# Performance work log

Hardware: AMD Instinct MI355X
Metric: run time of the kernel (lower is better)

Reference implementation:

```python
import jax, jax.numpy as jnp
import numpy as np

N_EMBED = 1024
HEAD_SIZE = 128
B, T = 8, 2048


def setup_inputs() -> dict:
    key = jax.random.key(0)
    kx, kk, kq, kv = jax.random.split(key, 4)
    x = jax.random.normal(kx, (B, T, N_EMBED), dtype=jnp.float32)
    Wk = jax.random.normal(kk, (N_EMBED, HEAD_SIZE), dtype=jnp.float32) * (N_EMBED ** -0.5)
    Wq = jax.random.normal(kq, (N_EMBED, HEAD_SIZE), dtype=jnp.float32) * (N_EMBED ** -0.5)
    Wv = jax.random.normal(kv, (N_EMBED, HEAD_SIZE), dtype=jnp.float32) * (N_EMBED ** -0.5)
    return {"x": x, "Wk": Wk, "Wq": Wq, "Wv": Wv}


def reference(x, Wk, Wq, Wv):
    # x: [B, T, C]; single-head causal attention, dropout rate 0 (identity)
    t = x.shape[1]
    k = jnp.einsum("btc,ch->bth", x, Wk)  # keys
    q = jnp.einsum("btc,ch->bth", x, Wq)  # queries
    v = jnp.einsum("btc,ch->bth", x, Wv)  # values
    scale = k.shape[-1] ** -0.5
    scores = jnp.einsum("bqh,bkh->bqk", q, k) * scale  # [B, T, T]
    causal = jnp.tril(jnp.ones((t, t), dtype=bool))
    scores = jnp.where(causal, scores, -jnp.inf)
    attn = jax.nn.softmax(scores, axis=-1)
    return jnp.einsum("bqk,bkh->bqh", attn, v)
```

## Files before the change

### kernel.cpp

```cpp
#include <hip/hip_runtime.h>
#include <hip/hip_bf16.h>
#include <math.h>

#define B_ 8
#define T_ 2048
#define C_ 1024
#define D_ 128
#define M_ (B_*T_)

typedef __attribute__((ext_vector_type(8))) short short8;
typedef __attribute__((ext_vector_type(4))) float floatx4;
typedef __hip_bfloat16 bf16;

#define QSCALE 0.12751744416218247f

__global__ __launch_bounds__(256) void cvt_w2_kernel(const float* __restrict__ Wq,
                                                     const float* __restrict__ Wk,
                                                     const float* __restrict__ Wv,
                                                     bf16* __restrict__ Wt) {
    __shared__ bf16 tl[64][136];
    const int t = threadIdx.x;
    const int k0 = blockIdx.x * 64, g = blockIdx.y;
    const float* W = (g == 0) ? Wq : (g == 1) ? Wk : Wv;
    {
        int k = t >> 2, n0 = (t & 3) * 32;
        const float* src = W + (size_t)(k0 + k) * 128 + n0;
#pragma unroll
        for (int j = 0; j < 4; ++j) {
            float4 v0 = *(const float4*)(src + j * 8);
            float4 v1 = *(const float4*)(src + j * 8 + 4);
            union { short8 s; __hip_bfloat162 h[4]; } u;
            __hip_bfloat162 h;
            h.x = __float2bfloat16(v0.x); h.y = __float2bfloat16(v0.y); u.h[0] = h;
            h.x = __float2bfloat16(v0.z); h.y = __float2bfloat16(v0.w); u.h[1] = h;
            h.x = __float2bfloat16(v1.x); h.y = __float2bfloat16(v1.y); u.h[2] = h;
            h.x = __float2bfloat16(v1.z); h.y = __float2bfloat16(v1.w); u.h[3] = h;
            *(short8*)&tl[k][n0 + j * 8] = u.s;
        }
    }
    __syncthreads();
    {
        int n = t >> 1, ko = (t & 1) * 32;
        union { short8 s[4]; bf16 e[32]; } u;
#pragma unroll
        for (int i = 0; i < 32; ++i) u.e[i] = tl[ko + i][n];
        bf16* dst = Wt + (size_t)g * 131072 + (size_t)n * 1024 + k0 + ko;
#pragma unroll
        for (int j = 0; j < 4; ++j) *(short8*)(dst + j * 8) = u.s[j];
    }
}

__global__ __launch_bounds__(256, 3) void proj4_kernel(const float* __restrict__ x,
                                                       const bf16* __restrict__ Wt,
                                                       bf16* __restrict__ Qb,
                                                       bf16* __restrict__ Kb,
                                                       bf16* __restrict__ Vt) {
    __shared__ bf16 la[64][72];
    __shared__ bf16 lb[256][72];
    const int t = threadIdx.x;
    const int wave = t >> 6, lane = t & 63;
    const int quad = lane >> 4, l15 = lane & 15;
    const int row0 = (blockIdx.x >> 1) * 64;
    const int path = blockIdx.x & 1;
    const int ar = t >> 2, ao = (t & 3) * 16;

    if (path == 0) {
        floatx4 acc[4][4];
#pragma unroll
        for (int m = 0; m < 4; ++m)
#pragma unroll
            for (int n = 0; n < 4; ++n) acc[m][n] = (floatx4)0.0f;

        for (int kc = 0; kc < 16; ++kc) {
            {
                const float* src = x + (size_t)(row0 + ar) * 1024 + kc * 64 + ao;
                float4 v0 = *(const float4*)src;
                float4 v1 = *(const float4*)(src + 4);
                float4 v2 = *(const float4*)(src + 8);
                float4 v3 = *(const float4*)(src + 12);
                union { short8 s; __hip_bfloat162 h[4]; } u0, u1;
                __hip_bfloat162 h;
                h.x = __float2bfloat16(v0.x); h.y = __float2bfloat16(v0.y); u0.h[0] = h;
                h.x = __float2bfloat16(v0.z); h.y = __float2bfloat16(v0.w); u0.h[1] = h;
                h.x = __float2bfloat16(v1.x); h.y = __float2bfloat16(v1.y); u0.h[2] = h;
                h.x = __float2bfloat16(v1.z); h.y = __float2bfloat16(v1.w); u0.h[3] = h;
                h.x = __float2bfloat16(v2.x); h.y = __float2bfloat16(v2.y); u1.h[0] = h;
                h.x = __float2bfloat16(v2.z); h.y = __float2bfloat16(v2.w); u1.h[1] = h;
                h.x = __float2bfloat16(v3.x); h.y = __float2bfloat16(v3.y); u1.h[2] = h;
                h.x = __float2bfloat16(v3.z); h.y = __float2bfloat16(v3.w); u1.h[3] = h;
                *(short8*)&la[ar][ao] = u0.s;
                *(short8*)&la[ar][ao + 8] = u1.s;
            }
#pragma unroll
            for (int j = 0; j < 8; ++j) {
                int c = t + j * 256;
                int rb = c >> 3, ob = (c & 7) * 8;
                int g = rb >> 7, n = rb & 127;
                *(short8*)&lb[rb][ob] = *(const short8*)(Wt + (size_t)g * 131072 + (size_t)n * 1024 + kc * 64 + ob);
            }
            __syncthreads();
#pragma unroll
            for (int dk = 0; dk < 2; ++dk) {
                short8 af[4], bff[4];
#pragma unroll
                for (int m = 0; m < 4; ++m) af[m] = *(const short8*)&la[m * 16 + l15][dk * 32 + quad * 8];
#pragma unroll
                for (int n = 0; n < 4; ++n) bff[n] = *(const short8*)&lb[wave * 64 + n * 16 + l15][dk * 32 + quad * 8];
#pragma unroll
                for (int m = 0; m < 4; ++m)
#pragma unroll
                    for (int n = 0; n < 4; ++n)
                        acc[m][n] = __builtin_amdgcn_mfma_f32_16x16x32_bf16(af[m], bff[n], acc[m][n], 0, 0, 0);
            }
            __syncthreads();
        }

        bf16* outp = (wave < 2) ? Qb : Kb;
        const float qs = (wave < 2) ? QSCALE : 1.0f;
        const int cb = (wave & 1) * 64;
#pragma unroll
        for (int m = 0; m < 4; ++m)
#pragma unroll
            for (int r = 0; r < 4; ++r) {
                int row = row0 + m * 16 + quad * 4 + r;
#pragma unroll
                for (int n = 0; n < 4; ++n)
                    outp[(size_t)row * 128 + cb + n * 16 + l15] = __float2bfloat16(acc[m][n][r] * qs);
            }
    } else {
        const int wr = wave >> 1, wc = wave & 1;
        floatx4 acc[2][4];
#pragma unroll
        for (int m = 0; m < 2; ++m)
#pragma unroll
            for (int n = 0; n < 4; ++n) acc[m][n] = (floatx4)0.0f;

        for (int kc = 0; kc < 16; ++kc) {
            {
                const float* src = x + (size_t)(row0 + ar) * 1024 + kc * 64 + ao;
                float4 v0 = *(const float4*)src;
                float4 v1 = *(const float4*)(src + 4);
                float4 v2 = *(const float4*)(src + 8);
                float4 v3 = *(const float4*)(src + 12);
                union { short8 s; __hip_bfloat162 h[4]; } u0, u1;
                __hip_bfloat162 h;
                h.x = __float2bfloat16(v0.x); h.y = __float2bfloat16(v0.y); u0.h[0] = h;
                h.x = __float2bfloat16(v0.z); h.y = __float2bfloat16(v0.w); u0.h[1] = h;
                h.x = __float2bfloat16(v1.x); h.y = __float2bfloat16(v1.y); u0.h[2] = h;
                h.x = __float2bfloat16(v1.z); h.y = __float2bfloat16(v1.w); u0.h[3] = h;
                h.x = __float2bfloat16(v2.x); h.y = __float2bfloat16(v2.y); u1.h[0] = h;
                h.x = __float2bfloat16(v2.z); h.y = __float2bfloat16(v2.w); u1.h[1] = h;
                h.x = __float2bfloat16(v3.x); h.y = __float2bfloat16(v3.y); u1.h[2] = h;
                h.x = __float2bfloat16(v3.z); h.y = __float2bfloat16(v3.w); u1.h[3] = h;
                *(short8*)&la[ar][ao] = u0.s;
                *(short8*)&la[ar][ao + 8] = u1.s;
            }
#pragma unroll
            for (int j = 0; j < 4; ++j) {
                int c = t + j * 256;
                int rb = c >> 3, ob = (c & 7) * 8;
                *(short8*)&lb[rb][ob] = *(const short8*)(Wt + 2 * 131072 + (size_t)rb * 1024 + kc * 64 + ob);
            }
            __syncthreads();
#pragma unroll
            for (int dk = 0; dk < 2; ++dk) {
                short8 af[2], bff[4];
#pragma unroll
                for (int m = 0; m < 2; ++m) af[m] = *(const short8*)&la[wr * 32 + m * 16 + l15][dk * 32 + quad * 8];
#pragma unroll
                for (int n = 0; n < 4; ++n) bff[n] = *(const short8*)&lb[wc * 64 + n * 16 + l15][dk * 32 + quad * 8];
#pragma unroll
                for (int m = 0; m < 2; ++m)
#pragma unroll
                    for (int n = 0; n < 4; ++n)
                        acc[m][n] = __builtin_amdgcn_mfma_f32_16x16x32_bf16(af[m], bff[n], acc[m][n], 0, 0, 0);
            }
            __syncthreads();
        }

        bf16* vtl = &lb[0][0];
#pragma unroll
        for (int m = 0; m < 2; ++m)
#pragma unroll
            for (int r = 0; r < 4; ++r) {
                int tt = wr * 32 + m * 16 + quad * 4 + r;
#pragma unroll
                for (int n = 0; n < 4; ++n)
                    vtl[tt * 136 + wc * 64 + n * 16 + l15] = __float2bfloat16(acc[m][n][r]);
            }
        __syncthreads();
        {
            int d = t >> 1, toff = (t & 1) * 32;
            union { short8 s[4]; bf16 e[32]; } u;
#pragma unroll
            for (int i = 0; i < 32; ++i) u.e[i] = vtl[(toff + i) * 136 + d];
            int bb = row0 >> 11, t0 = row0 & 2047;
            bf16* dst = Vt + (size_t)(bb * D_ + d) * T_ + t0 + toff;
#pragma unroll
            for (int j = 0; j < 4; ++j) *(short8*)(dst + j * 8) = u.s[j];
        }
    }
}

__global__ __launch_bounds__(256, 3) void flash_fm2_kernel(const bf16* __restrict__ Qb,
                                                           const bf16* __restrict__ Kb,
                                                           const bf16* __restrict__ Vt,
                                                           float* __restrict__ out,
                                                           bf16* __restrict__ Opart,
                                                           float* __restrict__ Lpart) {
    const int tile = blockIdx.x, seg = blockIdx.y, b = blockIdx.z;
    const int keys_total = (tile + 1) * 64;
    const int nseg = (keys_total + 255) >> 8;
    if (seg >= nseg) return;

    __shared__ bf16 lds_k[64][136];
    __shared__ bf16 lds_v[128][72];
    __shared__ bf16 lds_p[4][16][72];
    const int t = threadIdx.x;
    const int wave = t >> 6, lane = t & 63;
    const int quad = lane >> 4, l15 = lane & 15;
    const int q0 = tile * 64;
    const int k_start = seg << 8;
    const int k_end = min(k_start + 256, keys_total);
    const int nch = (k_end - k_start) >> 6;

    short8 qf[4];
    {
        int qm = q0 + wave * 16 + l15;
#pragma unroll
        for (int dk = 0; dk < 4; ++dk)
            qf[dk] = *(const short8*)(Qb + (size_t)(b * T_ + qm) * 128 + dk * 32 + quad * 8);
    }

    short8 kreg[4], vreg[4];
    {
        const int k0 = k_start;
#pragma unroll
        for (int j = 0; j < 4; ++j) {
            int c = t + j * 256;
            { int r = c >> 4, co = (c & 15) * 8;
              kreg[j] = *(const short8*)(Kb + (size_t)(b * T_ + k0 + r) * 128 + co); }
            { int d = c >> 3, co = (c & 7) * 8;
              vreg[j] = *(const short8*)(Vt + (size_t)b * (D_ * T_) + d * T_ + k0 + co); }
        }
    }

    floatx4 o_acc[8];
#pragma unroll
    for (int i = 0; i < 8; ++i) o_acc[i] = (floatx4)0.0f;
    float lp[4] = {0.f, 0.f, 0.f, 0.f};
    const int qrow = q0 + wave * 16 + quad * 4;

    for (int ch = 0; ch < nch; ++ch) {
        const int k0 = k_start + (ch << 6);
        __syncthreads();
#pragma unroll
        for (int j = 0; j < 4; ++j) {
            int c = t + j * 256;
            { int r = c >> 4, co = (c & 15) * 8; *(short8*)&lds_k[r][co] = kreg[j]; }
            { int d = c >> 3, co = (c & 7) * 8;  *(short8*)&lds_v[d][co] = vreg[j]; }
        }
        if (ch + 1 < nch) {
            const int kn = k0 + 64;
#pragma unroll
            for (int j = 0; j < 4; ++j) {
                int c = t + j * 256;
                { int r = c >> 4, co = (c & 15) * 8;
                  kreg[j] = *(const short8*)(Kb + (size_t)(b * T_ + kn + r) * 128 + co); }
                { int d = c >> 3, co = (c & 7) * 8;
                  vreg[j] = *(const short8*)(Vt + (size_t)b * (D_ * T_) + d * T_ + kn + co); }
            }
        }
        __syncthreads();

        floatx4 s[4];
#pragma unroll
        for (int nt = 0; nt < 4; ++nt) s[nt] = (floatx4)0.0f;
#pragma unroll
        for (int dk = 0; dk < 4; ++dk)
#pragma unroll
            for (int nt = 0; nt < 4; ++nt) {
                short8 kb = *(const short8*)&lds_k[nt * 16 + l15][dk * 32 + quad * 8];
                s[nt] = __builtin_amdgcn_mfma_f32_16x16x32_bf16(qf[dk], kb, s[nt], 0, 0, 0);
            }

        float sv[4][4];
#pragma unroll
        for (int nt = 0; nt < 4; ++nt)
#pragma unroll
            for (int r = 0; r < 4; ++r) sv[nt][r] = s[nt][r];

        if (k0 + 63 > q0) {
#pragma unroll
            for (int nt = 0; nt < 4; ++nt) {
                int key = k0 + nt * 16 + l15;
#pragma unroll
                for (int r = 0; r < 4; ++r)
                    if (key > qrow + r) sv[nt][r] = -1e30f;
            }
        }

#pragma unroll
        for (int nt = 0; nt < 4; ++nt)
#pragma unroll
            for (int r = 0; r < 4; ++r) sv[nt][r] = exp2f(sv[nt][r]);
#pragma unroll
        for (int r = 0; r < 4; ++r)
            lp[r] += (sv[0][r] + sv[1][r]) + (sv[2][r] + sv[3][r]);

#pragma unroll
        for (int nt = 0; nt < 4; ++nt)
#pragma unroll
            for (int r = 0; r < 4; ++r)
                lds_p[wave][quad * 4 + r][nt * 16 + l15] = __float2bfloat16(sv[nt][r]);
        short8 pa0 = *(const short8*)&lds_p[wave][l15][quad * 8];
        short8 pa1 = *(const short8*)&lds_p[wave][l15][32 + quad * 8];

#pragma unroll
        for (int nt = 0; nt < 8; ++nt) {
            short8 vb0 = *(const short8*)&lds_v[nt * 16 + l15][quad * 8];
            short8 vb1 = *(const short8*)&lds_v[nt * 16 + l15][32 + quad * 8];
            o_acc[nt] = __builtin_amdgcn_mfma_f32_16x16x32_bf16(pa0, vb0, o_acc[nt], 0, 0, 0);
            o_acc[nt] = __builtin_amdgcn_mfma_f32_16x16x32_bf16(pa1, vb1, o_acc[nt], 0, 0, 0);
        }
    }

    float l_i[4];
#pragma unroll
    for (int r = 0; r < 4; ++r) {
        float v = lp[r];
        v += __shfl_xor(v, 1);
        v += __shfl_xor(v, 2);
        v += __shfl_xor(v, 4);
        v += __shfl_xor(v, 8);
        l_i[r] = v;
    }

    const int lrow = wave * 16 + quad * 4;
    if (nseg == 1) {
        float inv_l[4];
#pragma unroll
        for (int r = 0; r < 4; ++r) inv_l[r] = 1.0f / l_i[r];
#pragma unroll
        for (int f = 0; f < 8; ++f)
#pragma unroll
            for (int r = 0; r < 4; ++r)
                out[(size_t)(b * T_ + qrow + r) * 128 + f * 16 + l15] = o_acc[f][r] * inv_l[r];
    } else {
        int pre = 0;
        for (int u = 4; u < tile; ++u) pre += (u + 4) >> 2;
        const size_t slot = (size_t)b * 140 + pre + seg;
        bf16* ob = Opart + slot * (64 * 128);
#pragma unroll
        for (int f = 0; f < 8; ++f)
#pragma unroll
            for (int r = 0; r < 4; ++r)
                ob[(size_t)(lrow + r) * 128 + f * 16 + l15] = __float2bfloat16(o_acc[f][r]);
        if (l15 == 0) {
#pragma unroll
            for (int r = 0; r < 4; ++r)
                Lpart[slot * 64 + lrow + r] = l_i[r];
        }
    }
}

__global__ __launch_bounds__(256) void combine4_kernel(const bf16* __restrict__ Opart,
                                                       const float* __restrict__ Lpart,
                                                       float* __restrict__ out) {
    const int tile = blockIdx.x + 4, b = blockIdx.y;
    const int nseg = (tile + 4) >> 2;
    int pre = 0;
    for (int u = 4; u < tile; ++u) pre += (u + 4) >> 2;
    const size_t slot0 = (size_t)b * 140 + pre;
    const int t = threadIdx.x;
    const int row = t >> 2, c0 = (t & 3) * 32;

    float lsum = 0.f;
    for (int j = 0; j < nseg; ++j) lsum += Lpart[(slot0 + j) * 64 + row];

    float acc[32];
#pragma unroll
    for (int i = 0; i < 32; ++i) acc[i] = 0.f;
    for (int j = 0; j < nseg; ++j) {
        const bf16* src = Opart + (slot0 + j) * (64 * 128) + (size_t)row * 128 + c0;
#pragma unroll
        for (int u = 0; u < 4; ++u) {
            short8 v8 = *(const short8*)(src + u * 8);
#pragma unroll
            for (int e = 0; e < 8; ++e) {
                union { unsigned int u32; float f; } cv;
                cv.u32 = ((unsigned int)(unsigned short)v8[e]) << 16;
                acc[u * 8 + e] += cv.f;
            }
        }
    }
    float inv = 1.0f / lsum;
    float* dst = out + (size_t)(b * T_ + tile * 64 + row) * 128 + c0;
#pragma unroll
    for (int i = 0; i < 32; ++i) dst[i] = acc[i] * inv;
}

extern "C" void kernel_launch(void* const* d_in, const int* in_sizes, int n_in,
                              void* d_out, int out_size, void* d_ws, size_t ws_size,
                              hipStream_t stream) {
    const float* x  = (const float*)d_in[0];
    const float* Wk = (const float*)d_in[1];
    const float* Wq = (const float*)d_in[2];
    const float* Wv = (const float*)d_in[3];
    float* out = (float*)d_out;

    char* ws = (char*)d_ws;
    bf16*  Wt    = (bf16*)ws;
    bf16*  Qb    = (bf16*)(ws + 786432);
    bf16*  Kb    = (bf16*)(ws + 4980736);
    bf16*  Vt    = (bf16*)(ws + 9175040);
    bf16*  Opart = (bf16*)(ws + 13369344);
    float* Lpart = (float*)(ws + 31719424);

    cvt_w2_kernel<<<dim3(16, 3), 256, 0, stream>>>(Wq, Wk, Wv, Wt);
    proj4_kernel<<<512, 256, 0, stream>>>(x, Wt, Qb, Kb, Vt);
    flash_fm2_kernel<<<dim3(32, 8, B_), 256, 0, stream>>>(Qb, Kb, Vt, out, Opart, Lpart);
    combine4_kernel<<<dim3(28, B_), 256, 0, stream>>>(Opart, Lpart, out);
}
```

Measured before the change: 85.86 us.

## Merge QK and V projection paths into one 512-thread block with register prefetch

The two block types of the projection kernel (Q/K path and V path, which each reread the same x rows) become one 512-thread block that computes all 384 output columns for its 64 rows, so each x tile is loaded and converted to bf16 only once. The next K-chunk of x and W is prefetched into registers while the current chunk is staged in LDS, so global loads overlap the MFMA work. In exchange the block uses more LDS and registers, and the grid shrinks to 256 blocks, which may leave some CUs with less parallel work.

Measured after the change: 82.16 us. 1.05x faster.

```diff
diff --git a/kernel.cpp b/kernel.cpp
--- a/kernel.cpp
+++ b/kernel.cpp
@@ -50,155 +50,113 @@
     }
 }
 
-__global__ __launch_bounds__(256, 3) void proj4_kernel(const float* __restrict__ x,
+__global__ __launch_bounds__(512, 2) void proj5_kernel(const float* __restrict__ x,
                                                        const bf16* __restrict__ Wt,
                                                        bf16* __restrict__ Qb,
                                                        bf16* __restrict__ Kb,
                                                        bf16* __restrict__ Vt) {
     __shared__ bf16 la[64][72];
-    __shared__ bf16 lb[256][72];
+    __shared__ bf16 lb[384][72];
     const int t = threadIdx.x;
     const int wave = t >> 6, lane = t & 63;
     const int quad = lane >> 4, l15 = lane & 15;
-    const int row0 = (blockIdx.x >> 1) * 64;
-    const int path = blockIdx.x & 1;
-    const int ar = t >> 2, ao = (t & 3) * 16;
-
-    if (path == 0) {
-        floatx4 acc[4][4];
-#pragma unroll
-        for (int m = 0; m < 4; ++m)
-#pragma unroll
-            for (int n = 0; n < 4; ++n) acc[m][n] = (floatx4)0.0f;
-
-        for (int kc = 0; kc < 16; ++kc) {
-            {
-                const float* src = x + (size_t)(row0 + ar) * 1024 + kc * 64 + ao;
-                float4 v0 = *(const float4*)src;
-                float4 v1 = *(const float4*)(src + 4);
-                float4 v2 = *(const float4*)(src + 8);
-                float4 v3 = *(const float4*)(src + 12);
-                union { short8 s; __hip_bfloat162 h[4]; } u0, u1;
-                __hip_bfloat162 h;
-                h.x = __float2bfloat16(v0.x); h.y = __float2bfloat16(v0.y); u0.h[0] = h;
-                h.x = __float2bfloat16(v0.z); h.y = __float2bfloat16(v0.w); u0.h[1] = h;
-                h.x = __float2bfloat16(v1.x); h.y = __float2bfloat16(v1.y); u0.h[2] = h;
-                h.x = __float2bfloat16(v1.z); h.y = __float2bfloat16(v1.w); u0.h[3] = h;
-                h.x = __float2bfloat16(v2.x); h.y = __float2bfloat16(v2.y); u1.h[0] = h;
-                h.x = __float2bfloat16(v2.z); h.y = __float2bfloat16(v2.w); u1.h[1] = h;
-                h.x = __float2bfloat16(v3.x); h.y = __float2bfloat16(v3.y); u1.h[2] = h;
-                h.x = __float2bfloat16(v3.z); h.y = __float2bfloat16(v3.w); u1.h[3] = h;
-                *(short8*)&la[ar][ao] = u0.s;
-                *(short8*)&la[ar][ao + 8] = u1.s;
-            }
-#pragma unroll
-            for (int j = 0; j < 8; ++j) {
-                int c = t + j * 256;
-                int rb = c >> 3, ob = (c & 7) * 8;
-                int g = rb >> 7, n = rb & 127;
-                *(short8*)&lb[rb][ob] = *(const short8*)(Wt + (size_t)g * 131072 + (size_t)n * 1024 + kc * 64 + ob);
-            }
-            __syncthreads();
-#pragma unroll
-            for (int dk = 0; dk < 2; ++dk) {
-                short8 af[4], bff[4];
-#pragma unroll
-                for (int m = 0; m < 4; ++m) af[m] = *(const short8*)&la[m * 16 + l15][dk * 32 + quad * 8];
-#pragma unroll
-                for (int n = 0; n < 4; ++n) bff[n] = *(const short8*)&lb[wave * 64 + n * 16 + l15][dk * 32 + quad * 8];
-#pragma unroll
-                for (int m = 0; m < 4; ++m)
-#pragma unroll
-                    for (int n = 0; n < 4; ++n)
-                        acc[m][n] = __builtin_amdgcn_mfma_f32_16x16x32_bf16(af[m], bff[n], acc[m][n], 0, 0, 0);
-            }
-            __syncthreads();
-        }
-
-        bf16* outp = (wave < 2) ? Qb : Kb;
-        const float qs = (wave < 2) ? QSCALE : 1.0f;
-        const int cb = (wave & 1) * 64;
-#pragma unroll
-        for (int m = 0; m < 4; ++m)
-#pragma unroll
-            for (int r = 0; r < 4; ++r) {
-                int row = row0 + m * 16 + quad * 4 + r;
-#pragma unroll
-                for (int n = 0; n < 4; ++n)
-                    outp[(size_t)row * 128 + cb + n * 16 + l15] = __float2bfloat16(acc[m][n][r] * qs);
-            }
-    } else {
-        const int wr = wave >> 1, wc = wave & 1;
-        floatx4 acc[2][4];
-#pragma unroll
-        for (int m = 0; m < 2; ++m)
-#pragma unroll
-            for (int n = 0; n < 4; ++n) acc[m][n] = (floatx4)0.0f;
-
-        for (int kc = 0; kc < 16; ++kc) {
-            {
-                const float* src = x + (size_t)(row0 + ar) * 1024 + kc * 64 + ao;
-                float4 v0 = *(const float4*)src;
-                float4 v1 = *(const float4*)(src + 4);
-                float4 v2 = *(const float4*)(src + 8);
-                float4 v3 = *(const float4*)(src + 12);
-                union { short8 s; __hip_bfloat162 h[4]; } u0, u1;
-                __hip_bfloat162 h;
-                h.x = __float2bfloat16(v0.x); h.y = __float2bfloat16(v0.y); u0.h[0] = h;
-                h.x = __float2bfloat16(v0.z); h.y = __float2bfloat16(v0.w); u0.h[1] = h;
-                h.x = __float2bfloat16(v1.x); h.y = __float2bfloat16(v1.y); u0.h[2] = h;
-                h.x = __float2bfloat16(v1.z); h.y = __float2bfloat16(v1.w); u0.h[3] = h;
-                h.x = __float2bfloat16(v2.x); h.y = __float2bfloat16(v2.y); u1.h[0] = h;
-                h.x = __float2bfloat16(v2.z); h.y = __float2bfloat16(v2.w); u1.h[1] = h;
-                h.x = __float2bfloat16(v3.x); h.y = __float2bfloat16(v3.y); u1.h[2] = h;
-                h.x = __float2bfloat16(v3.z); h.y = __float2bfloat16(v3.w); u1.h[3] = h;
-                *(short8*)&la[ar][ao] = u0.s;
-                *(short8*)&la[ar][ao + 8] = u1.s;
-            }
-#pragma unroll
-            for (int j = 0; j < 4; ++j) {
-                int c = t + j * 256;
-                int rb = c >> 3, ob = (c & 7) * 8;
-                *(short8*)&lb[rb][ob] = *(const short8*)(Wt + 2 * 131072 + (size_t)rb * 1024 + kc * 64 + ob);
-            }
-            __syncthreads();
-#pragma unroll
-            for (int dk = 0; dk < 2; ++dk) {
-                short8 af[2], bff[4];
-#pragma unroll
-                for (int m = 0; m < 2; ++m) af[m] = *(const short8*)&la[wr * 32 + m * 16 + l15][dk * 32 + quad * 8];
-#pragma unroll
-                for (int n = 0; n < 4; ++n) bff[n] = *(const short8*)&lb[wc * 64 + n * 16 + l15][dk * 32 + quad * 8];
-#pragma unroll
-                for (int m = 0; m < 2; ++m)
-#pragma unroll
-                    for (int n = 0; n < 4; ++n)
-                        acc[m][n] = __builtin_amdgcn_mfma_f32_16x16x32_bf16(af[m], bff[n], acc[m][n], 0, 0, 0);
-            }
-            __syncthreads();
-        }
-
-        bf16* vtl = &lb[0][0];
-#pragma unroll
-        for (int m = 0; m < 2; ++m)
-#pragma unroll
-            for (int r = 0; r < 4; ++r) {
-                int tt = wr * 32 + m * 16 + quad * 4 + r;
-#pragma unroll
-                for (int n = 0; n < 4; ++n)
-                    vtl[tt * 136 + wc * 64 + n * 16 + l15] = __float2bfloat16(acc[m][n][r]);
-            }
+    const int wr2 = wave >> 2, wc2 = wave & 3;
+    const int row0 = blockIdx.x * 64;
+    const int ar = t >> 3, ao = (t & 7) * 8;
+
+    floatx4 acc[2][6];
+#pragma unroll
+    for (int m = 0; m < 2; ++m)
+#pragma unroll
+        for (int n = 0; n < 6; ++n) acc[m][n] = (floatx4)0.0f;
+
+    float4 xr0, xr1;
+    short8 wreg[6];
+    {
+        const float* src = x + (size_t)(row0 + ar) * 1024 + ao;
+        xr0 = *(const float4*)src;
+        xr1 = *(const float4*)(src + 4);
+#pragma unroll
+        for (int j = 0; j < 6; ++j) {
+            int c = t + j * 512;
+            int rb = c >> 3, ob = (c & 7) * 8;
+            wreg[j] = *(const short8*)(Wt + (size_t)rb * 1024 + ob);
+        }
+    }
+
+    for (int kc = 0; kc < 16; ++kc) {
         __syncthreads();
         {
-            int d = t >> 1, toff = (t & 1) * 32;
-            union { short8 s[4]; bf16 e[32]; } u;
-#pragma unroll
-            for (int i = 0; i < 32; ++i) u.e[i] = vtl[(toff + i) * 136 + d];
-            int bb = row0 >> 11, t0 = row0 & 2047;
-            bf16* dst = Vt + (size_t)(bb * D_ + d) * T_ + t0 + toff;
-#pragma unroll
-            for (int j = 0; j < 4; ++j) *(short8*)(dst + j * 8) = u.s[j];
-        }
+            union { short8 s; __hip_bfloat162 h[4]; } u;
+            __hip_bfloat162 h;
+            h.x = __float2bfloat16(xr0.x); h.y = __float2bfloat16(xr0.y); u.h[0] = h;
+            h.x = __float2bfloat16(xr0.z); h.y = __float2bfloat16(xr0.w); u.h[1] = h;
+            h.x = __float2bfloat16(xr1.x); h.y = __float2bfloat16(xr1.y); u.h[2] = h;
+            h.x = __float2bfloat16(xr1.z); h.y = __float2bfloat16(xr1.w); u.h[3] = h;
+            *(short8*)&la[ar][ao] = u.s;
+        }
+#pragma unroll
+        for (int j = 0; j < 6; ++j) {
+            int c = t + j * 512;
+            int rb = c >> 3, ob = (c & 7) * 8;
+            *(short8*)&lb[rb][ob] = wreg[j];
+        }
+        if (kc < 15) {
+            const float* src = x + (size_t)(row0 + ar) * 1024 + (kc + 1) * 64 + ao;
+            xr0 = *(const float4*)src;
+            xr1 = *(const float4*)(src + 4);
+#pragma unroll
+            for (int j = 0; j < 6; ++j) {
+                int c = t + j * 512;
+                int rb = c >> 3, ob = (c & 7) * 8;
+                wreg[j] = *(const short8*)(Wt + (size_t)rb * 1024 + (kc + 1) * 64 + ob);
+            }
+        }
+        __syncthreads();
+#pragma unroll
+        for (int dk = 0; dk < 2; ++dk) {
+            short8 af[2], bff[6];
+#pragma unroll
+            for (int m = 0; m < 2; ++m) af[m] = *(const short8*)&la[wr2 * 32 + m * 16 + l15][dk * 32 + quad * 8];
+#pragma unroll
+            for (int n = 0; n < 6; ++n) bff[n] = *(const short8*)&lb[wc2 * 96 + n * 16 + l15][dk * 32 + quad * 8];
+#pragma unroll
+            for (int m = 0; m < 2; ++m)
+#pragma unroll
+                for (int n = 0; n < 6; ++n)
+                    acc[m][n] = __builtin_amdgcn_mfma_f32_16x16x32_bf16(af[m], bff[n], acc[m][n], 0, 0, 0);
+        }
+    }
+
+    __syncthreads();
+    bf16* vtl = &lb[0][0];
+#pragma unroll
+    for (int m = 0; m < 2; ++m)
+#pragma unroll
+        for (int r = 0; r < 4; ++r) {
+            const int tt = wr2 * 32 + m * 16 + quad * 4 + r;
+            const int row = row0 + tt;
+#pragma unroll
+            for (int n = 0; n < 6; ++n) {
+                const int colb = wc2 * 96 + n * 16;
+                const int g = colb >> 7;
+                const int lc = (colb & 127) + l15;
+                const float v = acc[m][n][r];
+                if (g == 0)      Qb[(size_t)row * 128 + lc] = __float2bfloat16(v * QSCALE);
+                else if (g == 1) Kb[(size_t)row * 128 + lc] = __float2bfloat16(v);
+                else             vtl[tt * 136 + lc] = __float2bfloat16(v);
+            }
+        }
+    __syncthreads();
+    {
+        int d = t >> 2, toff = (t & 3) * 16;
+        union { short8 s[2]; bf16 e[16]; } u;
+#pragma unroll
+        for (int i = 0; i < 16; ++i) u.e[i] = vtl[(toff + i) * 136 + d];
+        int bb = row0 >> 11, t0 = row0 & 2047;
+        bf16* dst = Vt + (size_t)(bb * D_ + d) * T_ + t0 + toff;
+        *(short8*)(dst)     = u.s[0];
+        *(short8*)(dst + 8) = u.s[1];
     }
 }
 
@@ -418,7 +376,7 @@
     float* Lpart = (float*)(ws + 31719424);
 
     cvt_w2_kernel<<<dim3(16, 3), 256, 0, stream>>>(Wq, Wk, Wv, Wt);
-    proj4_kernel<<<512, 256, 0, stream>>>(x, Wt, Qb, Kb, Vt);
+    proj5_kernel<<<256, 512, 0, stream>>>(x, Wt, Qb, Kb, Vt);
     flash_fm2_kernel<<<dim3(32, 8, B_), 256, 0, stream>>>(Qb, Kb, Vt, out, Opart, Lpart);
     combine4_kernel<<<dim3(28, B_), 256, 0, stream>>>(Opart, Lpart, out);
 }
```
